# Kernel tuning notes

Measured on AMD Instinct MI355X. Metric: run time of the kernel, lower is better.

## Reference

```python
import jax, jax.numpy as jnp
import numpy as np

T, N, G, H, E = 20, 256, 8, 128, 64
G2 = G * G


def setup_inputs() -> dict:
    key = jax.random.key(0)
    ks = jax.random.split(key, 16)
    scene = jax.random.normal(ks[0], (T, N, 3), dtype=jnp.float32)
    grids = (jax.random.uniform(ks[1], (T, N, N, G2)) < 0.05).astype(jnp.float32)
    hidden_states = jax.random.normal(ks[2], (N, H), dtype=jnp.float32) * 0.1
    cell_states = jax.random.normal(ks[3], (N, H), dtype=jnp.float32) * 0.1
    dimensions = jnp.array([640, 480], dtype=jnp.int64)
    s = lambda fan: 1.0 / np.sqrt(fan)
    W_in = jax.random.normal(ks[4], (E, 2), dtype=jnp.float32) * s(2)
    b_in = jnp.zeros((E,), dtype=jnp.float32)
    W_t = jax.random.normal(ks[5], (E, G2 * H), dtype=jnp.float32) * s(G2 * H)
    b_t = jnp.zeros((E,), dtype=jnp.float32)
    W_ih = jax.random.normal(ks[6], (4 * H, 2 * E), dtype=jnp.float32) * s(2 * E)
    b_ih = jnp.zeros((4 * H,), dtype=jnp.float32)
    W_hh = jax.random.normal(ks[7], (4 * H, H), dtype=jnp.float32) * s(H)
    b_hh = jnp.zeros((4 * H,), dtype=jnp.float32)
    W_out = jax.random.normal(ks[8], (5, H), dtype=jnp.float32) * s(H)
    b_out = jnp.zeros((5,), dtype=jnp.float32)
    return {"scene": scene, "grids": grids, "hidden_states": hidden_states,
            "cell_states": cell_states, "dimensions": dimensions,
            "W_in": W_in, "b_in": b_in, "W_t": W_t, "b_t": b_t,
            "W_ih": W_ih, "b_ih": b_ih, "W_hh": W_hh, "b_hh": b_hh,
            "W_out": W_out, "b_out": b_out}


def reference(scene, grids, hidden_states, cell_states, dimensions,
              W_in, b_in, W_t, b_t, W_ih, b_ih, W_hh, b_hh, W_out, b_out):
    # dimensions is unused by forward() (only by infer()), kept for signature fidelity.
    xy_seq = scene[:, :, 1:3]  # [T, N, 2]

    def step(carry, xs):
        h, c = carry                      # [N, H] each
        xy, grid = xs                     # [N, 2], [N, N, G2]
        # social pooling: for each ped p, grid[p]^T @ h  -> [G2, H]
        social = jnp.einsum('pog,oh->pgh', grid, h).reshape(grid.shape[0], G2 * H)
        inp_emb = jax.nn.relu(xy @ W_in.T + b_in)         # [N, E] (dropout in eval mode)
        ten_emb = jax.nn.relu(social @ W_t.T + b_t)       # [N, E]
        x = jnp.concatenate([inp_emb, ten_emb], axis=1)   # [N, 2E]
        gates = x @ W_ih.T + b_ih + h @ W_hh.T + b_hh     # [N, 4H]
        i, f, g, o = jnp.split(gates, 4, axis=1)          # PyTorch LSTMCell gate order
        c2 = jax.nn.sigmoid(f) * c + jax.nn.sigmoid(i) * jnp.tanh(g)
        h2 = jax.nn.sigmoid(o) * jnp.tanh(c2)
        out = h2 @ W_out.T + b_out                        # [N, 5]
        return (h2, c2), out

    (h_fin, c_fin), outputs = jax.lax.scan(step, (hidden_states, cell_states), (xy_seq, grids))
    return outputs, h_fin, c_fin
```

## Files before the change

kernel.cpp:

```cpp
#include <hip/hip_runtime.h>
#include <cstdint>
#include <cstddef>

#define T_STEPS 20
#define N_PED   256
#define NG      16384

__device__ __forceinline__ int swz64(int row, int k) {
    return row * 64 + ((((k >> 2) ^ (row & 15)) << 2) | (k & 3));
}

__device__ __forceinline__ void st_agent_f2(float* p, float a, float b) {
    union { float f[2]; unsigned long long u; } cv;
    cv.f[0] = a; cv.f[1] = b;
    __hip_atomic_store((unsigned long long*)p, cv.u, __ATOMIC_RELAXED,
                       __HIP_MEMORY_SCOPE_AGENT);
}
__device__ __forceinline__ void ld_agent_f4(const float* p, float4* out) {
    union { unsigned long long u[2]; float4 f; } cv;
    cv.u[0] = __hip_atomic_load((const unsigned long long*)p, __ATOMIC_RELAXED,
                                __HIP_MEMORY_SCOPE_AGENT);
    cv.u[1] = __hip_atomic_load((const unsigned long long*)p + 1, __ATOMIC_RELAXED,
                                __HIP_MEMORY_SCOPE_AGENT);
    *out = cv.f;
}
__device__ __forceinline__ float ld_agent_f(const float* p) {
    return __hip_atomic_load(p, __ATOMIC_RELAXED, __HIP_MEMORY_SCOPE_AGENT);
}

__device__ __forceinline__ void gbar(unsigned int* bar, unsigned int target) {
    __syncthreads();
    if (threadIdx.x == 0) {
        __hip_atomic_fetch_add(bar, 1u, __ATOMIC_RELAXED, __HIP_MEMORY_SCOPE_AGENT);
        while (__hip_atomic_load(bar, __ATOMIC_RELAXED, __HIP_MEMORY_SCOPE_AGENT) < target)
            __builtin_amdgcn_s_sleep(1);
    }
    __syncthreads();
}

__global__ __launch_bounds__(256) void kP(
    const float* __restrict__ scene, const float* __restrict__ hidden,
    const float* __restrict__ cell,  const float* __restrict__ W_in,
    const float* __restrict__ b_in,  const float* __restrict__ W_ih,
    const float* __restrict__ b_ih,  const float* __restrict__ b_hh,
    const float* __restrict__ W_hh,
    float* __restrict__ pg, float* __restrict__ h0, float* __restrict__ c0,
    float* __restrict__ W_ihT, float* __restrict__ W_hhT)
{
    int bid = blockIdx.x, tid = threadIdx.x;
    if (bid >= 1280) {
        int gid = (bid - 1280) * 256 + tid;
        for (int u = gid; u < 32768; u += 4096) {
            h0[u] = hidden[u];
            c0[u] = cell[u];
            int e = u >> 9, j = u & 511;
            W_ihT[u] = W_ih[j * 128 + 64 + e];
        }
        for (int u = gid; u < 65536; u += 4096) {
            int h = u >> 9, j = u & 511;
            W_hhT[u] = W_hh[j * 128 + h];
        }
        return;
    }
    __shared__ float ie[16 * 64];
    __shared__ float wih[128 * 65];
    int tb = bid >> 6;
    int p0 = ((bid >> 2) & 15) * 16;
    int j0 = (bid & 3) * 128;

    for (int k = 0; k < 8; ++k) {
        int fl = (tid + k * 256) * 4;
        int j_loc = fl >> 6, e0 = fl & 63;
        float4 v = *(const float4*)(W_ih + (size_t)(j0 + j_loc) * 128 + e0);
        wih[j_loc * 65 + e0 + 0] = v.x;
        wih[j_loc * 65 + e0 + 1] = v.y;
        wih[j_loc * 65 + e0 + 2] = v.z;
        wih[j_loc * 65 + e0 + 3] = v.w;
    }
    {
        int pp = tid >> 4, e0 = (tid & 15) * 4;
        size_t sbase = ((size_t)tb * N_PED + (p0 + pp)) * 3;
        float x = scene[sbase + 1];
        float y = scene[sbase + 2];
        #pragma unroll
        for (int i = 0; i < 4; ++i) {
            int e = e0 + i;
            float v = b_in[e] + x * W_in[e * 2 + 0] + y * W_in[e * 2 + 1];
            ie[pp * 64 + e] = v > 0.f ? v : 0.f;
        }
    }
    __syncthreads();
    for (int k = 0; k < 8; ++k) {
        int u = k * 256 + tid;
        int pp = u >> 7, j_loc = u & 127;
        int j = j0 + j_loc;
        float s = b_ih[j] + b_hh[j];
        #pragma unroll 8
        for (int e = 0; e < 64; ++e)
            s = fmaf(ie[pp * 64 + e], wih[j_loc * 65 + e], s);
        pg[((size_t)tb * N_PED + (p0 + pp)) * 512 + j] = s;
    }
}

__global__ __launch_bounds__(256) void kC(
    const float* __restrict__ grids, int* __restrict__ counts,
    unsigned short* __restrict__ gidx, unsigned int* __restrict__ bar)
{
    int r = blockIdx.x;
    int tid = threadIdx.x, lane = tid & 63, w = tid >> 6;
    if (r == 0 && tid == 0) *bar = 0u;
    __shared__ unsigned short st[4][1024];
    __shared__ int wcnts[4];
    const float* row = grids + (size_t)r * NG;
    int wcnt = 0;
    for (int rd = 0; rd < 16; ++rd) {
        int fb = w * 4096 + rd * 256 + lane * 4;
        float4 v = *(const float4*)(row + fb);
        #pragma unroll
        for (int c = 0; c < 4; ++c) {
            float val = (c == 0) ? v.x : (c == 1) ? v.y : (c == 2) ? v.z : v.w;
            unsigned long long m = __ballot(val != 0.0f);
            if (val != 0.0f) {
                int pos = wcnt + (int)__popcll(m & ((1ull << lane) - 1ull));
                st[w][pos] = (unsigned short)(fb + c);
            }
            wcnt += (int)__popcll(m);
        }
    }
    if (lane == 0) wcnts[w] = wcnt;
    __syncthreads();
    int base = 0;
    #pragma unroll
    for (int i = 0; i < 4; ++i) if (i < w) base += wcnts[i];
    for (int k = lane; k < wcnt; k += 64)
        gidx[(size_t)r * 1024 + base + k] = st[w][k];
    if (tid == 0) counts[r] = wcnts[0] + wcnts[1] + wcnts[2] + wcnts[3];
}

__global__ __launch_bounds__(512) void kStep(
    const int* __restrict__ counts, const unsigned short* __restrict__ gidx,
    const float* __restrict__ W_t,  const float* __restrict__ pg,
    const float* __restrict__ W_ihT, const float* __restrict__ W_hhT,
    const float* __restrict__ b_t,  const float* __restrict__ W_out,
    const float* __restrict__ b_out,
    float* __restrict__ hbuf, float* __restrict__ cbuf,
    float* __restrict__ A, float* __restrict__ out,
    unsigned int* __restrict__ bar)
{
    __shared__ float smem[16384];
    int bid = blockIdx.x, tid = threadIdx.x;
    int lane = tid & 63, w = tid >> 6;
    unsigned int barn = 0;

    for (int t = 0; t < T_STEPS; ++t) {
        const float* h  = hbuf + (t & 1) * 32768;
        const float* c  = cbuf + (t & 1) * 32768;
        float*       hn = hbuf + ((t + 1) & 1) * 32768;
        float*       cn = cbuf + ((t + 1) & 1) * 32768;

        {
            int o0 = (bid >> 6) * 64, g = bid & 63;
            #pragma unroll
            for (int i = 0; i < 8; ++i) {
                int u = i * 512 + tid;
                if (u < 2048) {
                    int kh = u >> 10, rem = u & 1023, r = rem >> 4, k4 = (rem & 15) * 4;
                    float4 v;
                    ld_agent_f4(h + (size_t)(o0 + r) * 128 + kh * 64 + k4, &v);
                    *(float4*)&smem[kh * 4096 + swz64(r, k4)] = v;
                } else {
                    int v2 = u - 2048;
                    int kh = v2 >> 10, rem = v2 & 1023, e = rem >> 4, k4 = (rem & 15) * 4;
                    float4 v = *(const float4*)(W_t + (size_t)e * 8192 + g * 128 + kh * 64 + k4);
                    *(float4*)&smem[8192 + kh * 4096 + swz64(e, k4)] = v;
                }
            }
            __syncthreads();
            int kh = w >> 2, wq = w & 3;
            int wrow = (wq >> 1) * 32, wcol = (wq & 1) * 32;
            int lr = (lane >> 3) * 4, lc = (lane & 7) * 4;
            const float* hsb = &smem[kh * 4096];
            const float* wtb = &smem[8192 + kh * 4096];
            float acc[4][4] = {};
            #pragma unroll
            for (int k4i = 0; k4i < 16; ++k4i) {
                int kd = k4i * 4;
                float4 a[4], b[4];
                #pragma unroll
                for (int i = 0; i < 4; ++i) a[i] = *(const float4*)&hsb[swz64(wrow + lr + i, kd)];
                #pragma unroll
                for (int j = 0; j < 4; ++j) b[j] = *(const float4*)&wtb[swz64(wcol + lc + j, kd)];
                #pragma unroll
                for (int i = 0; i < 4; ++i)
                    #pragma unroll
                    for (int j = 0; j < 4; ++j) {
                        acc[i][j] = fmaf(a[i].x, b[j].x, acc[i][j]);
                        acc[i][j] = fmaf(a[i].y, b[j].y, acc[i][j]);
                        acc[i][j] = fmaf(a[i].z, b[j].z, acc[i][j]);
                        acc[i][j] = fmaf(a[i].w, b[j].w, acc[i][j]);
                    }
            }
            __syncthreads();
            if (kh == 1) {
                #pragma unroll
                for (int i = 0; i < 4; ++i) {
                    int row = wrow + lr + i;
                    int col = (wcol + lc) ^ (((row >> 2) & 7) << 3);
                    *(float4*)&smem[row * 64 + col] =
                        make_float4(acc[i][0], acc[i][1], acc[i][2], acc[i][3]);
                }
            }
            __syncthreads();
            if (kh == 0) {
                #pragma unroll
                for (int i = 0; i < 4; ++i) {
                    int row = wrow + lr + i;
                    int col = (wcol + lc) ^ (((row >> 2) & 7) << 3);
                    float4 r4 = *(const float4*)&smem[row * 64 + col];
                    float* dst = &A[(size_t)(o0 + row) * 4096 + g * 64 + wcol + lc];
                    st_agent_f2(dst + 0, acc[i][0] + r4.x, acc[i][1] + r4.y);
                    st_agent_f2(dst + 2, acc[i][2] + r4.z, acc[i][3] + r4.w);
                }
            }
        }
        gbar(bar, 256u * (++barn));

        {
            int p = bid, r = t * N_PED + p;
            unsigned short* lidx = (unsigned short*)smem;
            float* part = smem + 512;
            float* ten  = smem + 1024;
            float* gts  = smem + 1088;
            float* h2s  = smem + 1600;
            float* hcur = smem + 1728;
            int cnt = counts[r];
            ((unsigned int*)lidx)[tid] = ((const unsigned int*)(gidx + (size_t)r * 1024))[tid];
            if (tid < 128) hcur[tid] = ld_agent_f(&h[p * 128 + tid]);
            __syncthreads();

            float acc = 0.f;
            int k = w;
            for (; k + 56 < cnt; k += 64) {
                int i0 = lidx[k],      i1 = lidx[k + 8],  i2 = lidx[k + 16], i3 = lidx[k + 24];
                int i4 = lidx[k + 32], i5 = lidx[k + 40], i6 = lidx[k + 48], i7 = lidx[k + 56];
                float a0 = ld_agent_f(&A[(size_t)i0 * 64 + lane]);
                float a1 = ld_agent_f(&A[(size_t)i1 * 64 + lane]);
                float a2 = ld_agent_f(&A[(size_t)i2 * 64 + lane]);
                float a3 = ld_agent_f(&A[(size_t)i3 * 64 + lane]);
                float a4 = ld_agent_f(&A[(size_t)i4 * 64 + lane]);
                float a5 = ld_agent_f(&A[(size_t)i5 * 64 + lane]);
                float a6 = ld_agent_f(&A[(size_t)i6 * 64 + lane]);
                float a7 = ld_agent_f(&A[(size_t)i7 * 64 + lane]);
                acc += a0 + a1; acc += a2 + a3; acc += a4 + a5; acc += a6 + a7;
            }
            for (; k < cnt; k += 8)
                acc += ld_agent_f(&A[(size_t)lidx[k] * 64 + lane]);
            part[w * 64 + lane] = acc;
            __syncthreads();

            if (tid < 64) {
                float s = b_t[tid];
                #pragma unroll
                for (int ww = 0; ww < 8; ++ww) s += part[ww * 64 + tid];
                ten[tid] = s > 0.f ? s : 0.f;
            }
            __syncthreads();

            {
                int j = tid;
                float gj = pg[(size_t)r * 512 + j];
                #pragma unroll 8
                for (int e = 0; e < 64; ++e)
                    gj = fmaf(ten[e], W_ihT[e * 512 + j], gj);
                #pragma unroll 8
                for (int hd = 0; hd < 128; ++hd)
                    gj = fmaf(hcur[hd], W_hhT[hd * 512 + j], gj);
                gts[j] = gj;
            }
            __syncthreads();

            if (tid < 128) {
                float ig = gts[tid], fg = gts[128 + tid], ggt = gts[256 + tid], og = gts[384 + tid];
                float si = 1.f / (1.f + expf(-ig));
                float sf = 1.f / (1.f + expf(-fg));
                float so = 1.f / (1.f + expf(-og));
                float cold = c[p * 128 + tid];
                float c2 = sf * cold + si * tanhf(ggt);
                float h2 = so * tanhf(c2);
                cn[p * 128 + tid] = c2;
                __hip_atomic_store(&hn[p * 128 + tid], h2, __ATOMIC_RELAXED,
                                   __HIP_MEMORY_SCOPE_AGENT);
                h2s[tid] = h2;
                if (t == T_STEPS - 1) {
                    out[25600 + p * 128 + tid] = h2;
                    out[58368 + p * 128 + tid] = c2;
                }
            }
            __syncthreads();

            if (w < 5) {
                float s = h2s[lane] * W_out[w * 128 + lane]
                        + h2s[lane + 64] * W_out[w * 128 + 64 + lane];
                #pragma unroll
                for (int off = 32; off > 0; off >>= 1) s += __shfl_xor(s, off);
                if (lane == 0) out[(size_t)r * 5 + w] = s + b_out[w];
            }
        }
        if (t != T_STEPS - 1) gbar(bar, 256u * (++barn));
    }
}

extern "C" void kernel_launch(void* const* d_in, const int* in_sizes, int n_in,
                              void* d_out, int out_size, void* d_ws, size_t ws_size,
                              hipStream_t stream) {
    (void)in_sizes; (void)n_in; (void)out_size; (void)ws_size;
    const float* scene  = (const float*)d_in[0];
    const float* grids  = (const float*)d_in[1];
    const float* hidden = (const float*)d_in[2];
    const float* cell   = (const float*)d_in[3];
    const float* W_in  = (const float*)d_in[5];
    const float* b_in  = (const float*)d_in[6];
    const float* W_t   = (const float*)d_in[7];
    const float* b_t   = (const float*)d_in[8];
    const float* W_ih  = (const float*)d_in[9];
    const float* b_ih  = (const float*)d_in[10];
    const float* W_hh  = (const float*)d_in[11];
    const float* b_hh  = (const float*)d_in[12];
    const float* W_out = (const float*)d_in[13];
    const float* b_out = (const float*)d_in[14];

    float* ws   = (float*)d_ws;
    float* hbuf = ws;
    float* cbuf = ws + 65536;
    float* A    = ws + 131072;
    float* pg   = ws + 1310720;
    float* WT   = ws + 3932160;
    int*   counts = (int*)(ws + 3964928);
    unsigned short* gidx = (unsigned short*)(ws + 3970048);
    float* W_hhT = ws + 6591488;
    unsigned int* bar = (unsigned int*)(ws + 6657152);
    float* outf = (float*)d_out;

    hipLaunchKernelGGL(kC, dim3(5120), dim3(256), 0, stream,
                       grids, counts, gidx, bar);
    hipLaunchKernelGGL(kP, dim3(1296), dim3(256), 0, stream,
                       scene, hidden, cell, W_in, b_in, W_ih, b_ih, b_hh, W_hh,
                       pg, hbuf, cbuf, WT, W_hhT);

    const int* counts_c = counts;
    const unsigned short* gidx_c = gidx;
    const float* WT_c = WT;
    const float* W_hhT_c = W_hhT;
    const float* pg_c = pg;
    void* args[] = {
        (void*)&counts_c, (void*)&gidx_c, (void*)&W_t, (void*)&pg_c,
        (void*)&WT_c, (void*)&W_hhT_c, (void*)&b_t, (void*)&W_out,
        (void*)&b_out, (void*)&hbuf, (void*)&cbuf, (void*)&A, (void*)&outf,
        (void*)&bar
    };
    hipLaunchCooperativeKernel((const void*)kStep, dim3(256), dim3(512),
                               args, 0, stream);
}
```

Measured before the change: 1.220 ms.

## Replace global grid barriers with per-block dataflow flags and double-buffered A

The two full-grid barriers per timestep are removed. Each block now publishes per-block flags when it finishes writing its slice of A or h, and consumers poll only the flags they depend on: the 64 h-row flags for the GEMM, and all 256 A flags before the gather. A is double-buffered so the next step's GEMM writes cannot race with slower blocks still reading the previous step. The W_t tile load is also issued before waiting on h so it overlaps the wait. The intent is to cut barrier latency and allow skew between blocks, at the cost of extra workspace and relaxed-ordering flag protocols whose memory-visibility correctness is delicate.

New measurement: 1.119 ms. 8.3% less time.

```diff
diff --git a/kernel.cpp b/kernel.cpp
--- a/kernel.cpp
+++ b/kernel.cpp
@@ -27,15 +27,11 @@
 __device__ __forceinline__ float ld_agent_f(const float* p) {
     return __hip_atomic_load(p, __ATOMIC_RELAXED, __HIP_MEMORY_SCOPE_AGENT);
 }
-
-__device__ __forceinline__ void gbar(unsigned int* bar, unsigned int target) {
-    __syncthreads();
-    if (threadIdx.x == 0) {
-        __hip_atomic_fetch_add(bar, 1u, __ATOMIC_RELAXED, __HIP_MEMORY_SCOPE_AGENT);
-        while (__hip_atomic_load(bar, __ATOMIC_RELAXED, __HIP_MEMORY_SCOPE_AGENT) < target)
-            __builtin_amdgcn_s_sleep(1);
-    }
-    __syncthreads();
+__device__ __forceinline__ unsigned ld_flag(const unsigned* p) {
+    return __hip_atomic_load(p, __ATOMIC_RELAXED, __HIP_MEMORY_SCOPE_AGENT);
+}
+__device__ __forceinline__ void st_flag(unsigned* p, unsigned v) {
+    __hip_atomic_store(p, v, __ATOMIC_RELAXED, __HIP_MEMORY_SCOPE_AGENT);
 }
 
 __global__ __launch_bounds__(256) void kP(
@@ -104,11 +100,13 @@
 
 __global__ __launch_bounds__(256) void kC(
     const float* __restrict__ grids, int* __restrict__ counts,
-    unsigned short* __restrict__ gidx, unsigned int* __restrict__ bar)
+    unsigned short* __restrict__ gidx,
+    unsigned int* __restrict__ Aflag, unsigned int* __restrict__ hflag)
 {
     int r = blockIdx.x;
     int tid = threadIdx.x, lane = tid & 63, w = tid >> 6;
-    if (r == 0 && tid == 0) *bar = 0u;
+    if (r == 0) Aflag[tid] = 0u;
+    if (r == 1) hflag[tid] = 0u;
     __shared__ unsigned short st[4][1024];
     __shared__ int wcnts[4];
     const float* row = grids + (size_t)r * NG;
@@ -144,36 +142,48 @@
     const float* __restrict__ b_t,  const float* __restrict__ W_out,
     const float* __restrict__ b_out,
     float* __restrict__ hbuf, float* __restrict__ cbuf,
-    float* __restrict__ A, float* __restrict__ out,
-    unsigned int* __restrict__ bar)
+    float* __restrict__ A0, float* __restrict__ A1,
+    float* __restrict__ out,
+    unsigned int* __restrict__ Aflag, unsigned int* __restrict__ hflag)
 {
     __shared__ float smem[16384];
     int bid = blockIdx.x, tid = threadIdx.x;
     int lane = tid & 63, w = tid >> 6;
-    unsigned int barn = 0;
 
     for (int t = 0; t < T_STEPS; ++t) {
         const float* h  = hbuf + (t & 1) * 32768;
         const float* c  = cbuf + (t & 1) * 32768;
         float*       hn = hbuf + ((t + 1) & 1) * 32768;
         float*       cn = cbuf + ((t + 1) & 1) * 32768;
+        float*       Acur = (t & 1) ? A1 : A0;
 
         {
             int o0 = (bid >> 6) * 64, g = bid & 63;
             #pragma unroll
-            for (int i = 0; i < 8; ++i) {
+            for (int i = 0; i < 4; ++i) {
                 int u = i * 512 + tid;
-                if (u < 2048) {
-                    int kh = u >> 10, rem = u & 1023, r = rem >> 4, k4 = (rem & 15) * 4;
-                    float4 v;
-                    ld_agent_f4(h + (size_t)(o0 + r) * 128 + kh * 64 + k4, &v);
-                    *(float4*)&smem[kh * 4096 + swz64(r, k4)] = v;
-                } else {
-                    int v2 = u - 2048;
-                    int kh = v2 >> 10, rem = v2 & 1023, e = rem >> 4, k4 = (rem & 15) * 4;
-                    float4 v = *(const float4*)(W_t + (size_t)e * 8192 + g * 128 + kh * 64 + k4);
-                    *(float4*)&smem[8192 + kh * 4096 + swz64(e, k4)] = v;
-                }
+                int kh = u >> 10, rem = u & 1023, e = rem >> 4, k4 = (rem & 15) * 4;
+                float4 v = *(const float4*)(W_t + (size_t)e * 8192 + g * 128 + kh * 64 + k4);
+                *(float4*)&smem[8192 + kh * 4096 + swz64(e, k4)] = v;
+            }
+            if (t > 0) {
+                if (w == 0) {
+                    unsigned tgt = (unsigned)t;
+                    while (1) {
+                        unsigned v = ld_flag(&hflag[o0 + lane]);
+                        if (__all(v >= tgt)) break;
+                        __builtin_amdgcn_s_sleep(1);
+                    }
+                }
+            }
+            __syncthreads();
+            #pragma unroll
+            for (int i = 0; i < 4; ++i) {
+                int u = i * 512 + tid;
+                int kh = u >> 10, rem = u & 1023, r = rem >> 4, k4 = (rem & 15) * 4;
+                float4 v;
+                ld_agent_f4(h + (size_t)(o0 + r) * 128 + kh * 64 + k4, &v);
+                *(float4*)&smem[kh * 4096 + swz64(r, k4)] = v;
             }
             __syncthreads();
             int kh = w >> 2, wq = w & 3;
@@ -217,13 +227,14 @@
                     int row = wrow + lr + i;
                     int col = (wcol + lc) ^ (((row >> 2) & 7) << 3);
                     float4 r4 = *(const float4*)&smem[row * 64 + col];
-                    float* dst = &A[(size_t)(o0 + row) * 4096 + g * 64 + wcol + lc];
+                    float* dst = &Acur[(size_t)(o0 + row) * 4096 + g * 64 + wcol + lc];
                     st_agent_f2(dst + 0, acc[i][0] + r4.x, acc[i][1] + r4.y);
                     st_agent_f2(dst + 2, acc[i][2] + r4.z, acc[i][3] + r4.w);
                 }
             }
-        }
-        gbar(bar, 256u * (++barn));
+            __syncthreads();
+            if (tid == 0) st_flag(&Aflag[bid], (unsigned)(t + 1));
+        }
 
         {
             int p = bid, r = t * N_PED + p;
@@ -235,6 +246,20 @@
             float* hcur = smem + 1728;
             int cnt = counts[r];
             ((unsigned int*)lidx)[tid] = ((const unsigned int*)(gidx + (size_t)r * 1024))[tid];
+            if (w == 0) {
+                unsigned tgt = (unsigned)(t + 1);
+                const unsigned* af = Aflag + lane * 4;
+                while (1) {
+                    unsigned v0 = ld_flag(af + 0), v1 = ld_flag(af + 1);
+                    unsigned v2 = ld_flag(af + 2), v3 = ld_flag(af + 3);
+                    unsigned m01 = v0 < v1 ? v0 : v1;
+                    unsigned m23 = v2 < v3 ? v2 : v3;
+                    unsigned mn  = m01 < m23 ? m01 : m23;
+                    if (__all(mn >= tgt)) break;
+                    __builtin_amdgcn_s_sleep(1);
+                }
+            }
+            __syncthreads();
             if (tid < 128) hcur[tid] = ld_agent_f(&h[p * 128 + tid]);
             __syncthreads();
 
@@ -243,18 +268,18 @@
             for (; k + 56 < cnt; k += 64) {
                 int i0 = lidx[k],      i1 = lidx[k + 8],  i2 = lidx[k + 16], i3 = lidx[k + 24];
                 int i4 = lidx[k + 32], i5 = lidx[k + 40], i6 = lidx[k + 48], i7 = lidx[k + 56];
-                float a0 = ld_agent_f(&A[(size_t)i0 * 64 + lane]);
-                float a1 = ld_agent_f(&A[(size_t)i1 * 64 + lane]);
-                float a2 = ld_agent_f(&A[(size_t)i2 * 64 + lane]);
-                float a3 = ld_agent_f(&A[(size_t)i3 * 64 + lane]);
-                float a4 = ld_agent_f(&A[(size_t)i4 * 64 + lane]);
-                float a5 = ld_agent_f(&A[(size_t)i5 * 64 + lane]);
-                float a6 = ld_agent_f(&A[(size_t)i6 * 64 + lane]);
-                float a7 = ld_agent_f(&A[(size_t)i7 * 64 + lane]);
+                float a0 = ld_agent_f(&Acur[(size_t)i0 * 64 + lane]);
+                float a1 = ld_agent_f(&Acur[(size_t)i1 * 64 + lane]);
+                float a2 = ld_agent_f(&Acur[(size_t)i2 * 64 + lane]);
+                float a3 = ld_agent_f(&Acur[(size_t)i3 * 64 + lane]);
+                float a4 = ld_agent_f(&Acur[(size_t)i4 * 64 + lane]);
+                float a5 = ld_agent_f(&Acur[(size_t)i5 * 64 + lane]);
+                float a6 = ld_agent_f(&Acur[(size_t)i6 * 64 + lane]);
+                float a7 = ld_agent_f(&Acur[(size_t)i7 * 64 + lane]);
                 acc += a0 + a1; acc += a2 + a3; acc += a4 + a5; acc += a6 + a7;
             }
             for (; k < cnt; k += 8)
-                acc += ld_agent_f(&A[(size_t)lidx[k] * 64 + lane]);
+                acc += ld_agent_f(&Acur[(size_t)lidx[k] * 64 + lane]);
             part[w * 64 + lane] = acc;
             __syncthreads();
 
@@ -297,6 +322,7 @@
                 }
             }
             __syncthreads();
+            if (tid == 0) st_flag(&hflag[bid], (unsigned)(t + 1));
 
             if (w < 5) {
                 float s = h2s[lane] * W_out[w * 128 + lane]
@@ -306,7 +332,6 @@
                 if (lane == 0) out[(size_t)r * 5 + w] = s + b_out[w];
             }
         }
-        if (t != T_STEPS - 1) gbar(bar, 256u * (++barn));
     }
 }
 
@@ -332,17 +357,19 @@
     float* ws   = (float*)d_ws;
     float* hbuf = ws;
     float* cbuf = ws + 65536;
-    float* A    = ws + 131072;
-    float* pg   = ws + 1310720;
-    float* WT   = ws + 3932160;
-    int*   counts = (int*)(ws + 3964928);
-    unsigned short* gidx = (unsigned short*)(ws + 3970048);
-    float* W_hhT = ws + 6591488;
-    unsigned int* bar = (unsigned int*)(ws + 6657152);
+    float* A0   = ws + 131072;
+    float* A1   = ws + 1179648;
+    float* pg   = ws + 2228224;
+    float* WT   = ws + 4849664;
+    float* W_hhT= ws + 4882432;
+    int*   counts = (int*)(ws + 4947968);
+    unsigned short* gidx = (unsigned short*)(ws + 4953088);
+    unsigned int* Aflag = (unsigned int*)(ws + 7574528);
+    unsigned int* hflag = (unsigned int*)(ws + 7574784);
     float* outf = (float*)d_out;
 
     hipLaunchKernelGGL(kC, dim3(5120), dim3(256), 0, stream,
-                       grids, counts, gidx, bar);
+                       grids, counts, gidx, Aflag, hflag);
     hipLaunchKernelGGL(kP, dim3(1296), dim3(256), 0, stream,
                        scene, hidden, cell, W_in, b_in, W_ih, b_ih, b_hh, W_hh,
                        pg, hbuf, cbuf, WT, W_hhT);
@@ -355,8 +382,8 @@
     void* args[] = {
         (void*)&counts_c, (void*)&gidx_c, (void*)&W_t, (void*)&pg_c,
         (void*)&WT_c, (void*)&W_hhT_c, (void*)&b_t, (void*)&W_out,
-        (void*)&b_out, (void*)&hbuf, (void*)&cbuf, (void*)&A, (void*)&outf,
-        (void*)&bar
+        (void*)&b_out, (void*)&hbuf, (void*)&cbuf, (void*)&A0, (void*)&A1,
+        (void*)&outf, (void*)&Aflag, (void*)&hflag
     };
     hipLaunchCooperativeKernel((const void*)kStep, dim3(256), dim3(512),
                                args, 0, stream);
```
